# Performance work log

Hardware: AMD Instinct MI355X
Metric: run time of the kernel (lower is better)

Reference implementation:

```python
import jax, jax.numpy as jnp
import numpy as np

N, E, F, T, C, HOR = 50000, 800000, 4, 12, 32, 12


def setup_inputs() -> dict:
    key = jax.random.key(0)
    ks = jax.random.split(key, 24)
    def rn(k, shape, s=0.1):
        return jax.random.normal(k, shape, jnp.float32) * s
    inp = {
        "x": jax.random.normal(ks[0], (N, F, T), jnp.float32),
        "edge_index": jax.random.randint(ks[1], (2, E), 0, N, dtype=jnp.int64),
        "edge_weight": jax.random.uniform(ks[2], (E,), jnp.float32),
        "attention": jax.random.uniform(ks[3], (T,), jnp.float32),
    }
    names = ["Wz", "bz", "Wlz", "blz", "Wr", "br", "Wlr", "blr", "Wh", "bh", "Wlh", "blh"]
    shapes = [(F, C), (C,), (2 * C, C), (C,), (F, C), (C,), (2 * C, C), (C,), (F, C), (C,), (2 * C, C), (C,)]
    for i, (n, s) in enumerate(zip(names, shapes)):
        inp[n] = rn(ks[4 + i], s)
    inp["Wout"] = rn(ks[20], (C, HOR))
    inp["bout"] = jnp.zeros((HOR,), jnp.float32)
    return inp


def reference(x, edge_index, edge_weight, attention,
              Wz, bz, Wlz, blz, Wr, br, Wlr, blr, Wh, bh, Wlh, blh,
              Wout, bout):
    n = x.shape[0]
    c = Wz.shape[1]
    row, col = edge_index[0], edge_index[1]

    # GCN normalization with self-loops (weight 1): A_hat = D^-1/2 (A+I) D^-1/2
    deg = jax.ops.segment_sum(edge_weight, col, num_segments=n) + 1.0
    dis = 1.0 / jnp.sqrt(deg)                      # deg >= 1 thanks to self-loop
    norm = dis[row] * edge_weight * dis[col]       # [E]
    self_norm = dis * dis                          # [N] self-loop coefficient

    def conv(xt, W, b):
        # xt: [N, F] -> [N, C]; sparse normalized aggregation over edge list
        xw = xt @ W
        agg = jax.ops.segment_sum(norm[:, None] * xw[row], col, num_segments=n)
        return agg + self_norm[:, None] * xw + b

    probs = jax.nn.softmax(attention)              # attention over periods
    H0 = jnp.zeros((n, c), x.dtype)                # A3TGCN passes H=None each period
    H_accum = jnp.zeros((n, c), x.dtype)
    for t in range(x.shape[2]):                    # fixed small period loop (as original)
        xt = x[:, :, t]
        Z = jax.nn.sigmoid(jnp.concatenate([conv(xt, Wz, bz), H0], axis=1) @ Wlz + blz)
        R = jax.nn.sigmoid(jnp.concatenate([conv(xt, Wr, br), H0], axis=1) @ Wlr + blr)
        Ht = jnp.tanh(jnp.concatenate([conv(xt, Wh, bh), H0 * R], axis=1) @ Wlh + blh)
        Hn = Z * H0 + (1.0 - Z) * Ht               # GRU update from zero state
        H_accum = H_accum + probs[t] * Hn

    h = jax.nn.relu(H_accum)
    return h @ Wout + bout
```

## Files before the change

### kernel.cpp

```cpp
#include <hip/hip_runtime.h>
#include <hip/hip_bf16.h>

#define NN 50000
#define NE 800000
#define FD 4
#define TD 12
#define CD 32
#define HD 12
#define FT 48
#define NBANK 8

#define OFF_HEAD   0
#define OFF_NEXT   400000
#define OFF_DIS    1200000
#define OFF_CST    1250000

__global__ void build_pre_kernel(const int* __restrict__ ei, int* __restrict__ head,
                                 int* __restrict__ next,
                                 const float* __restrict__ Wz, const float* __restrict__ bz,
                                 const float* __restrict__ Wlz, const float* __restrict__ blz,
                                 const float* __restrict__ Wh, const float* __restrict__ bh,
                                 const float* __restrict__ Wlh, const float* __restrict__ blh,
                                 const float* __restrict__ attention,
                                 float* __restrict__ cst) {
    int tid = threadIdx.x;
    if (blockIdx.x < (NE / 256)) {
        int e = blockIdx.x * 256 + tid;
        int c = ei[NE + e];
        int old = atomicExch(&head[(e & (NBANK-1)) * NN + c], e);
        next[e] = old;
        return;
    }
    if (tid < 128) {
        int f = tid >> 5, c = tid & 31;
        float s = 0.f, s2 = 0.f;
        #pragma unroll
        for (int k = 0; k < 32; ++k) {
            s  += Wz[f*32 + k] * Wlz[k*32 + c];
            s2 += Wh[f*32 + k] * Wlh[k*32 + c];
        }
        cst[tid]       = s;
        cst[160 + tid] = s2;
    } else if (tid < 160) {
        int c = tid - 128;
        float s = blz[c], s2 = blh[c];
        #pragma unroll
        for (int k = 0; k < 32; ++k) {
            s  += bz[k] * Wlz[k*32 + c];
            s2 += bh[k] * Wlh[k*32 + c];
        }
        cst[128 + c] = s;
        cst[288 + c] = s2;
    } else if (tid == 160) {
        float m = -1e30f;
        for (int t = 0; t < TD; ++t) m = fmaxf(m, attention[t]);
        float e[TD], s = 0.f;
        #pragma unroll
        for (int t = 0; t < TD; ++t) { e[t] = __expf(attention[t] - m); s += e[t]; }
        float inv = 1.f / s;
        #pragma unroll
        for (int t = 0; t < TD; ++t) cst[320 + t] = e[t] * inv;
    }
}

__global__ void degdis_kernel(const int* __restrict__ head, const int* __restrict__ next,
                              const float* __restrict__ w, float* __restrict__ dis) {
    int t = blockIdx.x * blockDim.x + threadIdx.x;
    int i = t >> 3;
    int b = t & 7;
    if (i >= NN) return;
    float s = 0.f;
    int e = head[b * NN + i];
    while (e >= 0) { s += w[e]; e = next[e]; }
    s += __shfl_xor(s, 1, 8);
    s += __shfl_xor(s, 2, 8);
    s += __shfl_xor(s, 4, 8);
    if (b == 0) dis[i] = rsqrtf(s + 1.0f);
}

__global__ __launch_bounds__(256) void gather_gru_kernel(
        const float4* __restrict__ x4, const float* __restrict__ dis,
        const int* __restrict__ head, const int* __restrict__ next,
        const int* __restrict__ ei, const float* __restrict__ w,
        const float* __restrict__ cst, const float* __restrict__ Wout,
        const float* __restrict__ bout, float* __restrict__ out) {
    __shared__ int2  smeta[16][64];
    __shared__ float sy[16][FT];
    __shared__ float hbuf[16][CD];
    __shared__ float sAz[128], sAh[128], sCz[32], sCh[32], sP[TD];
    __shared__ float sWout[CD * HD], sBout[HD];

    int tid = threadIdx.x;
    if (tid < 128) { sAz[tid] = cst[tid]; sAh[tid] = cst[160 + tid]; }
    if (tid < 32)  { sCz[tid] = cst[128 + tid]; sCh[tid] = cst[288 + tid]; }
    if (tid < TD)  { sP[tid] = cst[320 + tid]; sBout[tid] = bout[tid]; }
    for (int k = tid; k < CD * HD; k += 256) sWout[k] = Wout[k];
    __syncthreads();

    int g  = tid & 15;
    int ln = tid >> 4;
    int i  = blockIdx.x * 16 + ln;

    float d = dis[i];
    float4 a = (g < 12) ? x4[i * (FT/4) + g] : make_float4(0.f,0.f,0.f,0.f);
    float4 acc = make_float4(0.f, 0.f, 0.f, 0.f);

    int e = (g < 8) ? head[g * NN + i] : -1;

    while (true) {
        int r0=0,r1=0,r2=0,r3=0,r4=0,r5=0,r6=0,r7=0;
        float n0=0,n1=0,n2=0,n3=0,n4=0,n5=0,n6=0,n7=0;
        int cnt = 0;
        #define STEP(RK,NK) if (e >= 0) { RK = ei[e]; NK = dis[RK] * w[e]; e = next[e]; ++cnt; }
        STEP(r0,n0) STEP(r1,n1) STEP(r2,n2) STEP(r3,n3)
        STEP(r4,n4) STEP(r5,n5) STEP(r6,n6) STEP(r7,n7)
        #undef STEP

        int incl = cnt;
        #pragma unroll
        for (int dd = 1; dd < 8; dd <<= 1) {
            int t2 = __shfl_up(incl, dd, 16);
            if (g >= dd) incl += t2;
        }
        int S = __shfl(incl, 7, 16);
        if (S == 0) break;
        int off = incl - cnt;

        if (cnt > 0) smeta[ln][off + 0] = make_int2(r0, __float_as_int(n0));
        if (cnt > 1) smeta[ln][off + 1] = make_int2(r1, __float_as_int(n1));
        if (cnt > 2) smeta[ln][off + 2] = make_int2(r2, __float_as_int(n2));
        if (cnt > 3) smeta[ln][off + 3] = make_int2(r3, __float_as_int(n3));
        if (cnt > 4) smeta[ln][off + 4] = make_int2(r4, __float_as_int(n4));
        if (cnt > 5) smeta[ln][off + 5] = make_int2(r5, __float_as_int(n5));
        if (cnt > 6) smeta[ln][off + 6] = make_int2(r6, __float_as_int(n6));
        if (cnt > 7) smeta[ln][off + 7] = make_int2(r7, __float_as_int(n7));
        __builtin_amdgcn_wave_barrier();

        if (g < 12) {
            #pragma unroll 4
            for (int k = 0; k < S; ++k) {
                int2 m = smeta[ln][k];
                float nv = __int_as_float(m.y);
                float4 v = x4[m.x * (FT/4) + g];
                acc.x += nv * v.x; acc.y += nv * v.y;
                acc.z += nv * v.z; acc.w += nv * v.w;
            }
        }
    }

    if (g < 12) {
        float s0 = d * d;
        sy[ln][g*4 + 0] = a.x * s0 + d * acc.x;
        sy[ln][g*4 + 1] = a.y * s0 + d * acc.y;
        sy[ln][g*4 + 2] = a.z * s0 + d * acc.z;
        sy[ln][g*4 + 3] = a.w * s0 + d * acc.w;
    }
    __syncthreads();

    {
        int c0 = g, c1 = g + 16;
        float az00 = sAz[c0], az01 = sAz[32+c0], az02 = sAz[64+c0], az03 = sAz[96+c0];
        float az10 = sAz[c1], az11 = sAz[32+c1], az12 = sAz[64+c1], az13 = sAz[96+c1];
        float ah00 = sAh[c0], ah01 = sAh[32+c0], ah02 = sAh[64+c0], ah03 = sAh[96+c0];
        float ah10 = sAh[c1], ah11 = sAh[32+c1], ah12 = sAh[64+c1], ah13 = sAh[96+c1];
        float cz0 = sCz[c0], cz1 = sCz[c1], ch0 = sCh[c0], ch1 = sCh[c1];

        float hacc0 = 0.f, hacc1 = 0.f;
        #pragma unroll
        for (int t = 0; t < TD; ++t) {
            float y0 = sy[ln][0*TD + t];
            float y1 = sy[ln][1*TD + t];
            float y2 = sy[ln][2*TD + t];
            float y3 = sy[ln][3*TD + t];
            float z0 = cz0 + y0*az00 + y1*az01 + y2*az02 + y3*az03;
            float z1 = cz1 + y0*az10 + y1*az11 + y2*az12 + y3*az13;
            float h0 = ch0 + y0*ah00 + y1*ah01 + y2*ah02 + y3*ah03;
            float h1 = ch1 + y0*ah10 + y1*ah11 + y2*ah12 + y3*ah13;
            float Z0 = 1.f / (1.f + __expf(-z0));
            float Z1 = 1.f / (1.f + __expf(-z1));
            float e0 = __expf(2.f * h0);
            float e1 = __expf(2.f * h1);
            float H0v = (e0 - 1.f) / (e0 + 1.f);
            float H1v = (e1 - 1.f) / (e1 + 1.f);
            float p = sP[t];
            hacc0 += p * (1.f - Z0) * H0v;
            hacc1 += p * (1.f - Z1) * H1v;
        }
        hbuf[ln][c0] = fmaxf(hacc0, 0.f);
        hbuf[ln][c1] = fmaxf(hacc1, 0.f);
    }
    __syncthreads();

    if (tid < 16 * HD) {
        int lnode = tid / HD, hor = tid - lnode * HD;
        int gn = blockIdx.x * 16 + lnode;
        float s = sBout[hor];
        #pragma unroll
        for (int k = 0; k < CD; ++k) s += hbuf[lnode][k] * sWout[k * HD + hor];
        out[gn * HD + hor] = s;
    }
}

extern "C" void kernel_launch(void* const* d_in, const int* in_sizes, int n_in,
                              void* d_out, int out_size, void* d_ws, size_t ws_size,
                              hipStream_t stream) {
    const float* x      = (const float*)d_in[0];
    const int*   ei     = (const int*)d_in[1];
    const float* ew     = (const float*)d_in[2];
    const float* attn   = (const float*)d_in[3];
    const float* Wz     = (const float*)d_in[4];
    const float* bz     = (const float*)d_in[5];
    const float* Wlz    = (const float*)d_in[6];
    const float* blz    = (const float*)d_in[7];
    const float* Wh     = (const float*)d_in[12];
    const float* bh     = (const float*)d_in[13];
    const float* Wlh    = (const float*)d_in[14];
    const float* blh    = (const float*)d_in[15];
    const float* Wout   = (const float*)d_in[16];
    const float* bout   = (const float*)d_in[17];
    float* out = (float*)d_out;

    float* ws   = (float*)d_ws;
    int*   head = (int*)(ws + OFF_HEAD);
    int*   next = (int*)(ws + OFF_NEXT);
    float* dis  = ws + OFF_DIS;
    float* cst  = ws + OFF_CST;

    hipMemsetAsync(head, 0xFF, NBANK * NN * sizeof(int), stream);

    build_pre_kernel<<<NE / 256 + 1, 256, 0, stream>>>(ei, head, next,
                                                       Wz, bz, Wlz, blz,
                                                       Wh, bh, Wlh, blh, attn, cst);

    degdis_kernel<<<(NN * 8 + 255) / 256, 256, 0, stream>>>(head, next, ew, dis);

    gather_gru_kernel<<<NN / 16, 256, 0, stream>>>(
        (const float4*)x, dis, head, next, ei, ew, cst, Wout, bout, out);
}
```

Measured before the change: 212.8 us.

## Pack edge source, weight and next pointer into int4 payload; gather with float3 lanes

The build kernel now stores each edge's source row, weight and linked-list next pointer together in one 16-byte record. Degree and gather traversals then fetch a single int4 per edge instead of three scattered loads from ei, w and next. The feature gather also changes from 12 lanes reading float4 to all 16 lanes reading float3, spreading the 48 features across the full lane group. The cost is a larger workspace and extra write traffic in the build step, plus float3 loads that may not be 16-byte aligned.

Measured after the change: 198.2 us. 1.07x faster.

```diff
diff --git a/kernel.cpp b/kernel.cpp
--- a/kernel.cpp
+++ b/kernel.cpp
@@ -11,12 +11,12 @@
 #define NBANK 8
 
 #define OFF_HEAD   0
-#define OFF_NEXT   400000
-#define OFF_DIS    1200000
-#define OFF_CST    1250000
-
-__global__ void build_pre_kernel(const int* __restrict__ ei, int* __restrict__ head,
-                                 int* __restrict__ next,
+#define OFF_PAY    400000
+#define OFF_DIS    3600000
+#define OFF_CST    3650000
+
+__global__ void build_pre_kernel(const int* __restrict__ ei, const float* __restrict__ w,
+                                 int* __restrict__ head, int4* __restrict__ pay4,
                                  const float* __restrict__ Wz, const float* __restrict__ bz,
                                  const float* __restrict__ Wlz, const float* __restrict__ blz,
                                  const float* __restrict__ Wh, const float* __restrict__ bh,
@@ -26,9 +26,10 @@
     int tid = threadIdx.x;
     if (blockIdx.x < (NE / 256)) {
         int e = blockIdx.x * 256 + tid;
+        int r = ei[e];
         int c = ei[NE + e];
         int old = atomicExch(&head[(e & (NBANK-1)) * NN + c], e);
-        next[e] = old;
+        pay4[e] = make_int4(r, __float_as_int(w[e]), old, 0);
         return;
     }
     if (tid < 128) {
@@ -63,15 +64,19 @@
     }
 }
 
-__global__ void degdis_kernel(const int* __restrict__ head, const int* __restrict__ next,
-                              const float* __restrict__ w, float* __restrict__ dis) {
+__global__ void degdis_kernel(const int* __restrict__ head, const int4* __restrict__ pay4,
+                              float* __restrict__ dis) {
     int t = blockIdx.x * blockDim.x + threadIdx.x;
     int i = t >> 3;
     int b = t & 7;
     if (i >= NN) return;
     float s = 0.f;
     int e = head[b * NN + i];
-    while (e >= 0) { s += w[e]; e = next[e]; }
+    while (e >= 0) {
+        int4 p = pay4[e];
+        s += __int_as_float(p.y);
+        e = p.z;
+    }
     s += __shfl_xor(s, 1, 8);
     s += __shfl_xor(s, 2, 8);
     s += __shfl_xor(s, 4, 8);
@@ -79,9 +84,8 @@
 }
 
 __global__ __launch_bounds__(256) void gather_gru_kernel(
-        const float4* __restrict__ x4, const float* __restrict__ dis,
-        const int* __restrict__ head, const int* __restrict__ next,
-        const int* __restrict__ ei, const float* __restrict__ w,
+        const float* __restrict__ x, const float* __restrict__ dis,
+        const int* __restrict__ head, const int4* __restrict__ pay4,
         const float* __restrict__ cst, const float* __restrict__ Wout,
         const float* __restrict__ bout, float* __restrict__ out) {
     __shared__ int2  smeta[16][64];
@@ -101,9 +105,10 @@
     int ln = tid >> 4;
     int i  = blockIdx.x * 16 + ln;
 
+    const float3* x3 = (const float3*)x;
     float d = dis[i];
-    float4 a = (g < 12) ? x4[i * (FT/4) + g] : make_float4(0.f,0.f,0.f,0.f);
-    float4 acc = make_float4(0.f, 0.f, 0.f, 0.f);
+    float3 a = x3[i * 16 + g];
+    float ax = 0.f, ay = 0.f, az = 0.f;
 
     int e = (g < 8) ? head[g * NN + i] : -1;
 
@@ -111,7 +116,8 @@
         int r0=0,r1=0,r2=0,r3=0,r4=0,r5=0,r6=0,r7=0;
         float n0=0,n1=0,n2=0,n3=0,n4=0,n5=0,n6=0,n7=0;
         int cnt = 0;
-        #define STEP(RK,NK) if (e >= 0) { RK = ei[e]; NK = dis[RK] * w[e]; e = next[e]; ++cnt; }
+        #define STEP(RK,NK) if (e >= 0) { int4 p = pay4[e]; RK = p.x; \
+            NK = dis[p.x] * __int_as_float(p.y); e = p.z; ++cnt; }
         STEP(r0,n0) STEP(r1,n1) STEP(r2,n2) STEP(r3,n3)
         STEP(r4,n4) STEP(r5,n5) STEP(r6,n6) STEP(r7,n7)
         #undef STEP
@@ -136,24 +142,20 @@
         if (cnt > 7) smeta[ln][off + 7] = make_int2(r7, __float_as_int(n7));
         __builtin_amdgcn_wave_barrier();
 
-        if (g < 12) {
-            #pragma unroll 4
-            for (int k = 0; k < S; ++k) {
-                int2 m = smeta[ln][k];
-                float nv = __int_as_float(m.y);
-                float4 v = x4[m.x * (FT/4) + g];
-                acc.x += nv * v.x; acc.y += nv * v.y;
-                acc.z += nv * v.z; acc.w += nv * v.w;
-            }
-        }
-    }
-
-    if (g < 12) {
+        #pragma unroll 8
+        for (int k = 0; k < S; ++k) {
+            int2 m = smeta[ln][k];
+            float nv = __int_as_float(m.y);
+            float3 v = x3[m.x * 16 + g];
+            ax += nv * v.x; ay += nv * v.y; az += nv * v.z;
+        }
+    }
+
+    {
         float s0 = d * d;
-        sy[ln][g*4 + 0] = a.x * s0 + d * acc.x;
-        sy[ln][g*4 + 1] = a.y * s0 + d * acc.y;
-        sy[ln][g*4 + 2] = a.z * s0 + d * acc.z;
-        sy[ln][g*4 + 3] = a.w * s0 + d * acc.w;
+        sy[ln][g*3 + 0] = a.x * s0 + d * ax;
+        sy[ln][g*3 + 1] = a.y * s0 + d * ay;
+        sy[ln][g*3 + 2] = a.z * s0 + d * az;
     }
     __syncthreads();
 
@@ -222,18 +224,18 @@
 
     float* ws   = (float*)d_ws;
     int*   head = (int*)(ws + OFF_HEAD);
-    int*   next = (int*)(ws + OFF_NEXT);
+    int4*  pay4 = (int4*)(ws + OFF_PAY);
     float* dis  = ws + OFF_DIS;
     float* cst  = ws + OFF_CST;
 
     hipMemsetAsync(head, 0xFF, NBANK * NN * sizeof(int), stream);
 
-    build_pre_kernel<<<NE / 256 + 1, 256, 0, stream>>>(ei, head, next,
+    build_pre_kernel<<<NE / 256 + 1, 256, 0, stream>>>(ei, ew, head, pay4,
                                                        Wz, bz, Wlz, blz,
                                                        Wh, bh, Wlh, blh, attn, cst);
 
-    degdis_kernel<<<(NN * 8 + 255) / 256, 256, 0, stream>>>(head, next, ew, dis);
+    degdis_kernel<<<(NN * 8 + 255) / 256, 256, 0, stream>>>(head, pay4, dis);
 
     gather_gru_kernel<<<NN / 16, 256, 0, stream>>>(
-        (const float4*)x, dis, head, next, ei, ew, cst, Wout, bout, out);
-}
+        x, dis, head, pay4, cst, Wout, bout, out);
+}
```
